# Kernel tuning notes

Hardware: AMD Instinct MI355X
Metric: run time of the kernel (lower is better)

The kernel has to match this reference:

```python
import jax, jax.numpy as jnp
import numpy as np

D = 64        # embedding_dim
H = 16        # embedding_dim // 4
DAY = 86400.0
N_USERS = 200000
T_TOTAL = 8400000


def _mlp(x, w1, b1, w2, b2):
    return jax.nn.relu(x @ w1 + b1) @ w2 + b2


def setup_inputs() -> dict:
    key = jax.random.key(0)
    ks = jax.random.split(key, 20)
    N, T = N_USERS, T_TOTAL
    # every user gets >= 3 check-ins, rest assigned randomly
    base = np.tile(np.arange(N, dtype=np.int32), 3)
    rnd = np.asarray(jax.random.randint(ks[0], (T - 3 * N,), 0, N, dtype=jnp.int32))
    segment_ids = jnp.asarray(np.sort(np.concatenate([base, rnd])).astype(np.int32))
    # quantized coordinates so per-user unique-row counting is meaningful
    locations = jnp.round(jax.random.normal(ks[1], (T, 2), jnp.float32) * 50.0) / 50.0
    timestamps = jax.random.uniform(ks[2], (T,), jnp.float32, 0.0, 1.0e7)
    categories = jax.random.randint(ks[3], (T,), 0, 10, dtype=jnp.int32)

    def lin(k, din, dout):
        kw, kb = jax.random.split(k)
        w = jax.random.normal(kw, (din, dout), jnp.float32) / np.float32(np.sqrt(din))
        b = jax.random.normal(kb, (dout,), jnp.float32) * 0.01
        return w, b

    p = {}
    ki = 4
    for nm, din in [("loc", 2), ("tmp", 3), ("act", 10), ("mob", 4)]:
        p[f"w_{nm}1"], p[f"b_{nm}1"] = lin(ks[ki], din, H); ki += 1
        p[f"w_{nm}2"], p[f"b_{nm}2"] = lin(ks[ki], H, H); ki += 1
    p["w_cmb1"], p["b_cmb1"] = lin(ks[ki], D, D); ki += 1
    p["w_cmb2"], p["b_cmb2"] = lin(ks[ki], D, D)
    return dict(locations=locations, timestamps=timestamps,
                categories=categories, segment_ids=segment_ids, num_users=N, **p)


def reference(locations, timestamps,
              w_loc1, b_loc1, w_loc2, b_loc2,
              w_tmp1, b_tmp1, w_tmp2, b_tmp2,
              w_act1, b_act1, w_act2, b_act2,
              w_mob1, b_mob1, w_mob2, b_mob2,
              w_cmb1, b_cmb1, w_cmb2, b_cmb2,
              categories, segment_ids, num_users):
    seg, N = segment_ids, num_users
    ss = lambda v: jax.ops.segment_sum(v, seg, num_segments=N, indices_are_sorted=True)
    L = ss(jnp.ones_like(timestamps))                        # [N] check-ins per user

    # home location = mean over user's locations
    home = ss(locations) / L[:, None]                        # [N, 2]

    # temporal patterns: mean hour / day / month
    hours = jnp.mod(timestamps, DAY) / 3600.0
    days = jnp.mod(timestamps / DAY, 7.0)
    months = jnp.mod(timestamps / (30.0 * DAY), 12.0)
    tmp = ss(jnp.stack([hours, days, months], -1)) / L[:, None]   # [N, 3]

    # activity distribution over 10 POI categories
    hist = jnp.zeros((N, 10), locations.dtype).at[seg, categories].add(1.0)
    hs = hist.sum(-1, keepdims=True)
    act = jnp.where(hs > 0, hist / jnp.maximum(hs, 1.0), hist)    # [N, 10]

    # mobility stats: radius = std (ddof=1) of distance to centroid
    d = jnp.linalg.norm(locations - home[seg], axis=1)
    dmean = ss(d) / L
    radius = jnp.sqrt(ss((d - dmean[seg]) ** 2) / (L - 1.0))

    # diversity: unique locations per user via segment-local lexsort
    x, y = locations[:, 0], locations[:, 1]
    order = jnp.lexsort((y, x, seg))
    sx, sy, sseg = x[order], y[order], seg[order]
    new = jnp.concatenate([jnp.ones((1,), bool),
                           (sseg[1:] != sseg[:-1]) | (sx[1:] != sx[:-1]) | (sy[1:] != sy[:-1])])
    uniq = jax.ops.segment_sum(new.astype(locations.dtype), sseg,
                               num_segments=N, indices_are_sorted=True)
    diversity = uniq / L

    # frequency: check-ins per day of time span
    tmax = jax.ops.segment_max(timestamps, seg, num_segments=N, indices_are_sorted=True)
    tmin = jax.ops.segment_min(timestamps, seg, num_segments=N, indices_are_sorted=True)
    span = (tmax - tmin) / DAY
    freq = L / jnp.maximum(span, 1.0)

    # regularity: 1 / (std(consecutive time diffs, ddof=1) + 1e-6)
    diffs = timestamps[1:] - timestamps[:-1]
    same = seg[1:] == seg[:-1]
    seg1 = seg[1:]
    ss1 = lambda v: jax.ops.segment_sum(v, seg1, num_segments=N, indices_are_sorted=True)
    m = L - 1.0                                              # diffs per user
    dmu = ss1(jnp.where(same, diffs, 0.0)) / m
    dvar = ss1(jnp.where(same, (diffs - dmu[seg1]) ** 2, 0.0)) / (m - 1.0)
    reg = 1.0 / (jnp.sqrt(dvar) + 1e-6)

    mob = jnp.stack([radius, diversity, freq, reg], -1)      # [N, 4]

    feats = jnp.concatenate([
        _mlp(home, w_loc1, b_loc1, w_loc2, b_loc2),
        _mlp(tmp, w_tmp1, b_tmp1, w_tmp2, b_tmp2),
        _mlp(act, w_act1, b_act1, w_act2, b_act2),
        _mlp(mob, w_mob1, b_mob1, w_mob2, b_mob2),
    ], -1)                                                   # [N, 64]
    return _mlp(feats, w_cmb1, b_cmb1, w_cmb2, b_cmb2)       # [N, 64]
```

## Files before the change

kernel.cpp:

```cpp
#include <hip/hip_runtime.h>

typedef short bf16x8 __attribute__((ext_vector_type(8)));
typedef float f32x4 __attribute__((ext_vector_type(4)));

struct Params {
  const float* loc; const float* ts; const int* cat; const int* seg;
  const int* off;
  const float *wl1,*bl1,*wl2,*bl2;
  const float *wt1,*bt1,*wt2,*bt2;
  const float *wa1,*ba1,*wa2,*ba2;
  const float *wm1,*bm1,*wm2,*bm2;
  const float *wc1,*bc1,*wc2,*bc2;
  float* out;
  unsigned* wfrag;
  int N, T, use_off;
};

__global__ void offsets_kernel(const int* __restrict__ seg, int* __restrict__ off, int T, int N) {
  int i = blockIdx.x * blockDim.x + threadIdx.x;
  if (i == 0) off[N] = T;
  if (i < T) {
    int s = seg[i];
    if (i == 0 || seg[i-1] != s) off[s] = i;
  }
}

__device__ __forceinline__ int rdlane_i(int v, int l) {
  return __builtin_amdgcn_readlane(v, l);
}

__device__ __forceinline__ unsigned bf16r(float f) {
  unsigned x = __float_as_uint(f);
  return (x + 0x7fffu + ((x >> 16) & 1u)) >> 16;
}
__device__ __forceinline__ unsigned pack_hl(float f) {
  unsigned hi = bf16r(f);
  float r = f - __uint_as_float(hi << 16);
  return (hi << 16) | bf16r(r);
}

__device__ __forceinline__ float exact_fmod(float a, float m, float rcp_m) {
  float q = floorf(a * rcp_m);
  float r = fmaf(q, -m, a);
  if (r < 0.0f) r += m;
  else if (r >= m) r -= m;
  return r;
}

__device__ __forceinline__ f32x4 mfma16(bf16x8 a, bf16x8 b, f32x4 c) {
  return __builtin_amdgcn_mfma_f32_16x16x32_bf16(a, b, c, 0, 0, 0);
}

__device__ __forceinline__ void lda(const unsigned* rp, bf16x8& hi, bf16x8& lo) {
  uint4 w0 = *(const uint4*)rp;
  uint4 w1 = *(const uint4*)(rp + 4);
  union { unsigned u[4]; bf16x8 v; } H, L;
  H.u[0] = __builtin_amdgcn_perm(w0.y, w0.x, 0x07060302u);
  H.u[1] = __builtin_amdgcn_perm(w0.w, w0.z, 0x07060302u);
  H.u[2] = __builtin_amdgcn_perm(w1.y, w1.x, 0x07060302u);
  H.u[3] = __builtin_amdgcn_perm(w1.w, w1.z, 0x07060302u);
  L.u[0] = __builtin_amdgcn_perm(w0.y, w0.x, 0x05040100u);
  L.u[1] = __builtin_amdgcn_perm(w0.w, w0.z, 0x05040100u);
  L.u[2] = __builtin_amdgcn_perm(w1.y, w1.x, 0x05040100u);
  L.u[3] = __builtin_amdgcn_perm(w1.w, w1.z, 0x05040100u);
  hi = H.v; lo = L.v;
}

__device__ __forceinline__ float bdval_(const float* wl2, const float* wt2,
                                        const float* wa2, const float* wm2,
                                        int k, int col) {
  if ((k >> 4) != (col >> 4)) return 0.f;
  int b = col >> 4;
  const float* W2 = (b & 2) ? ((b & 1) ? wm2 : wa2) : ((b & 1) ? wt2 : wl2);
  return W2[(k & 15) * 16 + (col & 15)];
}

__device__ __forceinline__ unsigned frag_word(const Params& p, int m) {
  int fi = m >> 8;
  int ln = (m >> 2) & 63;
  int j2 = m & 3;
  int layer, nt, ks;
  if (fi < 4)       { layer = 0; nt = fi;             ks = nt >> 1; }
  else if (fi < 12) { layer = 1; nt = (fi - 4) >> 1;  ks = (fi - 4) & 1; }
  else              { layer = 2; nt = (fi - 12) >> 1; ks = (fi - 12) & 1; }
  int col = nt * 16 + (ln & 15);
  int k0  = ks * 32 + ((ln >> 4) << 3) + (j2 << 1);
  float v0, v1;
  if (layer == 0) {
    v0 = bdval_(p.wl2, p.wt2, p.wa2, p.wm2, k0, col);
    v1 = bdval_(p.wl2, p.wt2, p.wa2, p.wm2, k0 + 1, col);
  } else {
    const float* W = (layer == 1) ? p.wc1 : p.wc2;
    v0 = W[k0 * 64 + col]; v1 = W[(k0 + 1) * 64 + col];
  }
  return (bf16r(v1) << 16) | bf16r(v0);
}

__global__ void pack_kernel(Params p) {
  int m = blockIdx.x * 256 + threadIdx.x;
  if (m < 5120) p.wfrag[m] = frag_word(p, m);
}

__device__ __forceinline__ bf16x8 g_ldb(const Params& p, int fi, int lane) {
  union { uint4 q; unsigned u[4]; bf16x8 v; } U;
  if (p.wfrag) {
    U.q = *(const uint4*)(p.wfrag + ((fi * 64 + lane) << 2));
  } else {
    int m = fi * 256 + lane * 4;
    U.u[0] = frag_word(p, m + 0);
    U.u[1] = frag_word(p, m + 1);
    U.u[2] = frag_word(p, m + 2);
    U.u[3] = frag_word(p, m + 3);
  }
  return U.v;
}

__device__ __forceinline__ int lower_bound(const int* seg, int T, int v) {
  int lo = 0, hi = T;
  while (lo < hi) { int m = (lo + hi) >> 1; if (seg[m] < v) lo = m + 1; else hi = m; }
  return lo;
}

__device__ __forceinline__ float pscan_f(float v) {
  v += __int_as_float(__builtin_amdgcn_update_dpp(0, __float_as_int(v), 0x111, 0xf, 0xf, true));
  v += __int_as_float(__builtin_amdgcn_update_dpp(0, __float_as_int(v), 0x112, 0xf, 0xf, true));
  v += __int_as_float(__builtin_amdgcn_update_dpp(0, __float_as_int(v), 0x114, 0xf, 0xf, true));
  v += __int_as_float(__builtin_amdgcn_update_dpp(0, __float_as_int(v), 0x118, 0xf, 0xf, true));
  v += __int_as_float(__builtin_amdgcn_update_dpp(0, __float_as_int(v), 0x142, 0xa, 0xf, true));
  v += __int_as_float(__builtin_amdgcn_update_dpp(0, __float_as_int(v), 0x143, 0xc, 0xf, true));
  return v;
}
__device__ __forceinline__ unsigned pscan_u(unsigned v) {
  int x = (int)v;
  x += __builtin_amdgcn_update_dpp(0, x, 0x111, 0xf, 0xf, true);
  x += __builtin_amdgcn_update_dpp(0, x, 0x112, 0xf, 0xf, true);
  x += __builtin_amdgcn_update_dpp(0, x, 0x114, 0xf, 0xf, true);
  x += __builtin_amdgcn_update_dpp(0, x, 0x118, 0xf, 0xf, true);
  x += __builtin_amdgcn_update_dpp(0, x, 0x142, 0xa, 0xf, true);
  x += __builtin_amdgcn_update_dpp(0, x, 0x143, 0xc, 0xf, true);
  return (unsigned)x;
}
__device__ __forceinline__ unsigned wshr1_u(unsigned v) {
  return (unsigned)__builtin_amdgcn_update_dpp(0, (int)v, 0x138, 0xf, 0xf, true);
}
__device__ __forceinline__ float wshr1_f(float v) {
  return __int_as_float(__builtin_amdgcn_update_dpp(0, __float_as_int(v), 0x138, 0xf, 0xf, true));
}

#define DPPI0(v, ctrl, rm) __builtin_amdgcn_update_dpp(0, (v), ctrl, rm, 0xf, true)
#define DPPFO(v, o, ctrl, rm) __int_as_float(__builtin_amdgcn_update_dpp(__float_as_int(o), __float_as_int(v), ctrl, rm, 0xf, false))

struct Conds { bool c1,c2,c4,c8,cA,cB; };
__device__ __forceinline__ Conds mkconds(int lane, int dist) {
  Conds C;
  C.c1 = dist >= 1; C.c2 = dist >= 2; C.c4 = dist >= 4; C.c8 = dist >= 8;
  C.cA = ((lane & 15) + 1) <= dist;
  C.cB = (lane - 31) <= dist;
  return C;
}
__device__ __forceinline__ int smaxi(int v) {
  int i;
  i = DPPI0(v,0x111,0xf); v = max(v,i);
  i = DPPI0(v,0x112,0xf); v = max(v,i);
  i = DPPI0(v,0x114,0xf); v = max(v,i);
  i = DPPI0(v,0x118,0xf); v = max(v,i);
  i = DPPI0(v,0x142,0xa); v = max(v,i);
  i = DPPI0(v,0x143,0xc); v = max(v,i);
  return v;
}
__device__ __forceinline__ float smaxf(float v, const Conds& C) {
  const float NI = __int_as_float(0xff800000u);
  float i;
  i = DPPFO(v,NI,0x111,0xf); v = C.c1 ? fmaxf(v,i) : v;
  i = DPPFO(v,NI,0x112,0xf); v = C.c2 ? fmaxf(v,i) : v;
  i = DPPFO(v,NI,0x114,0xf); v = C.c4 ? fmaxf(v,i) : v;
  i = DPPFO(v,NI,0x118,0xf); v = C.c8 ? fmaxf(v,i) : v;
  i = DPPFO(v,NI,0x142,0xa); v = C.cA ? fmaxf(v,i) : v;
  i = DPPFO(v,NI,0x143,0xc); v = C.cB ? fmaxf(v,i) : v;
  return v;
}
__device__ __forceinline__ float sminf(float v, const Conds& C) {
  const float PI_ = __int_as_float(0x7f800000u);
  float i;
  i = DPPFO(v,PI_,0x111,0xf); v = C.c1 ? fminf(v,i) : v;
  i = DPPFO(v,PI_,0x112,0xf); v = C.c2 ? fminf(v,i) : v;
  i = DPPFO(v,PI_,0x114,0xf); v = C.c4 ? fminf(v,i) : v;
  i = DPPFO(v,PI_,0x118,0xf); v = C.c8 ? fminf(v,i) : v;
  i = DPPFO(v,PI_,0x142,0xa); v = C.cA ? fminf(v,i) : v;
  i = DPPFO(v,PI_,0x143,0xc); v = C.cB ? fminf(v,i) : v;
  return v;
}

__global__ __launch_bounds__(256, 4) void mobility_kernel(Params p) {
  __shared__ __align__(16) unsigned s_pool[4352];
  __shared__ float s_w1[304];
  __shared__ float s_b1[64], s_b2[64], s_bc1[64], s_bc2[64];

  int tid = threadIdx.x;
  int lane = tid & 63, w = tid >> 6;

  if (tid < 32)  s_w1[tid]       = p.wl1[tid];
  if (tid < 48)  s_w1[32 + tid]  = p.wt1[tid];
  if (tid < 160) s_w1[80 + tid]  = p.wa1[tid];
  if (tid < 64)  s_w1[240 + tid] = p.wm1[tid];
  if (tid < 16) {
    s_b1[tid]    = p.bl1[tid]; s_b1[16+tid] = p.bt1[tid];
    s_b1[32+tid] = p.ba1[tid]; s_b1[48+tid] = p.bm1[tid];
    s_b2[tid]    = p.bl2[tid]; s_b2[16+tid] = p.bt2[tid];
    s_b2[32+tid] = p.ba2[tid]; s_b2[48+tid] = p.bm2[tid];
  }
  if (tid < 64) { s_bc1[tid] = p.bc1[tid]; s_bc2[tid] = p.bc2[tid]; }
  __syncthreads();

  int uw0 = blockIdx.x * 64 + w * 16;
  if (uw0 >= p.N) return;
  int myu = uw0 + lane;
  int myuc = min(myu, p.N - 1);
  int s0, e0;
  if (p.use_off) {
    s0 = p.off[myuc]; e0 = p.off[myuc + 1];
  } else {
    s0 = lower_bound(p.seg, p.T, myuc);
    e0 = lower_bound(p.seg, p.T, myuc + 1);
  }
  int W0 = rdlane_i(s0, 0);
  int W1 = rdlane_i(e0, 15);
  float Lf = (float)(e0 - s0);

  const float2* lp2 = (const float2*)p.loc;
  const float NINF = __int_as_float(0xff800000u);
  const float PINF = __int_as_float(0x7f800000u);

  int aKx = 0, aKy = 0, aXX = 0;
  float aH = 0.f, aDY = 0.f, aT = 0.f, aDF2 = 0.f;
  unsigned aH0 = 0u, aH1 = 0u, aH2 = 0u;
  float aTMX = NINF, aTMN = PINF;

  for (int base = W0; base < W1; base += 64) {
    int e = base + lane;
    bool on = e < W1;
    int ec = on ? e : (W1 - 1);
    int sv = p.seg[ec];
    int sp = (ec > 0) ? p.seg[ec - 1] : -1;
    int sn = (ec + 1 < p.T) ? p.seg[ec + 1] : -2;
    float t  = p.ts[ec];
    float tnx = (ec + 1 < p.T) ? p.ts[ec + 1] : 0.f;
    int c = p.cat[ec];
    float2 xy = lp2[ec];

    unsigned vXY = 0u, vXX = 0u, vH0 = 0u, vH1 = 0u, vH2 = 0u;
    float vH = 0.f, vDY = 0.f, vT = 0.f, vDF2 = 0.f;
    float vtmx = NINF, vtmn = PINF;
    if (on) {
      int kx = (int)lrintf(xy.x * 50.0f);
      int ky = (int)lrintf(xy.y * 50.0f);
      vXY = ((unsigned)(kx + 512) << 16) | (unsigned)(ky + 512);
      vXX = (unsigned)(kx * kx + ky * ky);
      float hr = exact_fmod(t, 86400.0f, 1.0f / 86400.0f);
      vH = hr * (1.0f / 3600.0f);
      float ud = (float)((double)t * (1.0 / 86400.0));
      vDY = exact_fmod(ud, 7.0f, 1.0f / 7.0f);
      vT = t;
      unsigned bit = 1u << ((c & 3) * 8);
      int wsel = c >> 2;
      vH0 = (wsel == 0) ? bit : 0u;
      vH1 = (wsel == 1) ? bit : 0u;
      vH2 = (wsel == 2) ? bit : 0u;
      if (sn == sv) { float dt = tnx - t; vDF2 = dt * dt; }
      vtmx = t; vtmn = t;
    }

    unsigned pXY = pscan_u(vXY), pXX = pscan_u(vXX);
    unsigned pH0 = pscan_u(vH0), pH1 = pscan_u(vH1), pH2 = pscan_u(vH2);
    float pH = pscan_f(vH), pDY = pscan_f(vDY), pT = pscan_f(vT), pDF2 = pscan_f(vDF2);

    bool head = (!on) || (sp != sv);
    int j = smaxi(head ? lane : 0);
    Conds C = mkconds(lane, lane - j);
    float pTMX = smaxf(vtmx, C);
    float pTMN = sminf(vtmn, C);

    int lo = min(max(s0 - base, 0), 64);
    int hi = min(max(e0 - base, 0), 64);
    int idx = max(hi - 1, 0);
    unsigned PXY = (unsigned)__shfl((int)pXY, idx);
    unsigned PXX = (unsigned)__shfl((int)pXX, idx);
    unsigned PH0 = (unsigned)__shfl((int)pH0, idx);
    unsigned PH1 = (unsigned)__shfl((int)pH1, idx);
    unsigned PH2 = (unsigned)__shfl((int)pH2, idx);
    float PH = __shfl(pH, idx), PDY = __shfl(pDY, idx);
    float PT = __shfl(pT, idx), PDF2 = __shfl(pDF2, idx);
    float PTMX = __shfl(pTMX, idx), PTMN = __shfl(pTMN, idx);
    unsigned LXY = wshr1_u(PXY), LXX = wshr1_u(PXX);
    unsigned LH0 = wshr1_u(PH0), LH1 = wshr1_u(PH1), LH2 = wshr1_u(PH2);
    float LH = wshr1_f(PH), LDY = wshr1_f(PDY);
    float LT = wshr1_f(PT), LDF2 = wshr1_f(PDF2);

    if (hi > lo) {
      int cnt = hi - lo;
      bool ul_ = lo > 0;
      unsigned dXY = PXY - (ul_ ? LXY : 0u);
      aKx += (int)(dXY >> 16) - (cnt << 9);
      aKy += (int)(dXY & 0xffffu) - (cnt << 9);
      aXX += (int)(PXX - (ul_ ? LXX : 0u));
      aH0 += PH0 - (ul_ ? LH0 : 0u);
      aH1 += PH1 - (ul_ ? LH1 : 0u);
      aH2 += PH2 - (ul_ ? LH2 : 0u);
      aH   += PH   - (ul_ ? LH   : 0.f);
      aDY  += PDY  - (ul_ ? LDY  : 0.f);
      aT   += PT   - (ul_ ? LT   : 0.f);
      aDF2 += PDF2 - (ul_ ? LDF2 : 0.f);
      aTMX = fmaxf(aTMX, PTMX);
      aTMN = fminf(aTMN, PTMN);
    }
  }

  float hx, hy;
  {
    float sx = (float)aKx / 50.0f, sy = (float)aKy / 50.0f;
    hx = sx / Lf; hy = sy / Lf;
  }

  float aD = 0.f;
  for (int base = W0; base < W1; base += 64) {
    int e = base + lane;
    bool on = e < W1;
    int ec = on ? e : (W1 - 1);
    int sv = p.seg[ec];
    float2 xy = lp2[ec];
    int ul = sv - uw0;
    float hxu = __shfl(hx, ul), hyu = __shfl(hy, ul);
    float d = 0.f;
    if (on) {
      float dx = xy.x - hxu, dyv = xy.y - hyu;
      d = sqrtf(fmaf(dx, dx, dyv * dyv));
    }
    float pD = pscan_f(d);
    int lo = min(max(s0 - base, 0), 64);
    int hi = min(max(e0 - base, 0), 64);
    int idx = max(hi - 1, 0);
    float PD = __shfl(pD, idx);
    float LD = wshr1_f(PD);
    if (hi > lo) aD += PD - ((lo > 0) ? LD : 0.f);
  }

  unsigned* fw = s_pool + w * 1088;
  unsigned* hashp = fw;
  float uqf = 0.f;
  for (int uu = 0; uu < 16; ++uu) {
    if (uw0 + uu >= p.N) break;
    int suu = rdlane_i(s0, uu), euu = rdlane_i(e0, uu);
    int Lu = euu - suu;
    int uq = 0;
    if (Lu <= 96) {
      hashp[lane] = 0u; hashp[64 + lane] = 0u;
      asm volatile("s_waitcnt lgkmcnt(0)" ::: "memory");
      for (int b2 = suu; b2 < euu; b2 += 64) {
        int i = b2 + lane;
        bool fresh = false;
        if (i < euu) {
          float2 xy = lp2[i];
          int kx = (int)lrintf(xy.x * 50.0f) + 2048;
          int ky = (int)lrintf(xy.y * 50.0f) + 2048;
          unsigned key = (((unsigned)kx << 12) | (unsigned)ky) + 1u;
          unsigned h = (key * 2654435761u) >> 25;
          while (true) {
            unsigned old = atomicCAS(&hashp[h], 0u, key);
            if (old == 0u) { fresh = true; break; }
            if (old == key) break;
            h = (h + 1) & 127u;
          }
        }
        uq += (int)__popcll(__ballot(fresh));
      }
    } else {
      for (int b2 = suu; b2 < euu; b2 += 64) {
        int i = b2 + lane;
        bool fresh = false;
        if (i < euu) {
          float x = p.loc[2*(size_t)i], y = p.loc[2*(size_t)i+1];
          fresh = true;
          for (int jj = suu; jj < i; ++jj) {
            if (p.loc[2*(size_t)jj] == x && p.loc[2*(size_t)jj+1] == y) { fresh = false; break; }
          }
        }
        uq += (int)__popcll(__ballot(fresh));
      }
    }
    if (lane == uu) uqf = (float)uq;
  }
  asm volatile("s_waitcnt lgkmcnt(0)" ::: "memory");

  int lr = lane & 15, g2 = lane >> 4;
  int us0 = __shfl(s0, lr), ue0 = __shfl(e0, lr);
  float LfU = (float)(ue0 - us0);
  int KX = __shfl(aKx, lr), KY = __shfl(aKy, lr), XX = __shfl(aXX, lr);
  float H_ = __shfl(aH, lr), DY_ = __shfl(aDY, lr);
  float T_ = __shfl(aT, lr), DF2_ = __shfl(aDF2, lr);
  unsigned H0_ = (unsigned)__shfl((int)aH0, lr);
  unsigned H1_ = (unsigned)__shfl((int)aH1, lr);
  unsigned H2_ = (unsigned)__shfl((int)aH2, lr);
  float TMX_ = __shfl(aTMX, lr), TMN_ = __shfl(aTMN, lr);
  float D_ = __shfl(aD, lr), UQ_ = __shfl(uqf, lr);

  unsigned hp16[16];
  if (g2 == 0) {
    float sxU = (float)KX / 50.0f, syU = (float)KY / 50.0f;
    float hxU = sxU / LfU, hyU = syU / LfU;
    #pragma unroll
    for (int j = 0; j < 16; ++j)
      hp16[j] = pack_hl(fmaxf(s_b1[j] + hxU * s_w1[j] + hyU * s_w1[16 + j], 0.f));
  } else if (g2 == 1) {
    float th = H_ / LfU, tdy = DY_ / LfU;
    float tmo = (T_ * (1.0f / 2592000.0f)) / LfU;
    #pragma unroll
    for (int j = 0; j < 16; ++j)
      hp16[j] = pack_hl(fmaxf(s_b1[16 + j] + th * s_w1[32 + j] + tdy * s_w1[48 + j]
                              + tmo * s_w1[64 + j], 0.f));
  } else if (g2 == 2) {
    float act[10];
    act[0] = (float)(H0_ & 255u) / LfU;
    act[1] = (float)((H0_ >> 8) & 255u) / LfU;
    act[2] = (float)((H0_ >> 16) & 255u) / LfU;
    act[3] = (float)((H0_ >> 24) & 255u) / LfU;
    act[4] = (float)(H1_ & 255u) / LfU;
    act[5] = (float)((H1_ >> 8) & 255u) / LfU;
    act[6] = (float)((H1_ >> 16) & 255u) / LfU;
    act[7] = (float)((H1_ >> 24) & 255u) / LfU;
    act[8] = (float)(H2_ & 255u) / LfU;
    act[9] = (float)((H2_ >> 8) & 255u) / LfU;
    #pragma unroll
    for (int j = 0; j < 16; ++j) {
      float aa = s_b1[32 + j];
      #pragma unroll
      for (int b = 0; b < 10; ++b) aa = fmaf(act[b], s_w1[80 + b * 16 + j], aa);
      hp16[j] = pack_hl(fmaxf(aa, 0.f));
    }
  } else {
    float sxU = (float)KX / 50.0f, syU = (float)KY / 50.0f;
    float sxx = (float)XX / 2500.0f;
    float sD = D_;
    float sD2 = sxx - (sxU * sxU + syU * syU) / LfU;
    float varD = (sD2 - sD * sD / LfU) / (LfU - 1.0f);
    float rad  = sqrtf(fmaxf(varD, 0.0f));
    float divy = UQ_ / LfU;
    float span = (TMX_ - TMN_) / 86400.0f;
    float freq = LfU / fmaxf(span, 1.0f);
    float tfirst = p.ts[us0];
    float tlast  = p.ts[ue0 - 1];
    float sdf = tlast - tfirst;
    float mm   = LfU - 1.0f;
    float dmu  = sdf / mm;
    float dvar = (DF2_ - mm * dmu * dmu) / (mm - 1.0f);
    float reg  = 1.0f / (sqrtf(fmaxf(dvar, 0.0f)) + 1e-6f);
    #pragma unroll
    for (int j = 0; j < 16; ++j)
      hp16[j] = pack_hl(fmaxf(s_b1[48 + j] + rad * s_w1[240 + j] + divy * s_w1[256 + j]
                              + freq * s_w1[272 + j] + reg * s_w1[288 + j], 0.f));
  }

  {
    unsigned* row = fw + lr * 68 + g2 * 16;
    #pragma unroll
    for (int j = 0; j < 4; ++j)
      *(uint4*)(row + 4 * j) = make_uint4(hp16[4*j], hp16[4*j+1], hp16[4*j+2], hp16[4*j+3]);
  }
  asm volatile("s_waitcnt lgkmcnt(0)" ::: "memory");

  int lg = lane >> 4;
  const unsigned* arow = fw + lr * 68 + (lg << 3);

  bf16x8 ah[2], al[2];
  lda(arow,      ah[0], al[0]);
  lda(arow + 32, ah[1], al[1]);
  f32x4 acc[4];
  #pragma unroll
  for (int nt = 0; nt < 4; ++nt) {
    float bv = s_b2[nt * 16 + lr];
    acc[nt] = (f32x4){bv, bv, bv, bv};
    int ks = nt >> 1;
    bf16x8 bw = g_ldb(p, nt, lane);
    acc[nt] = mfma16(ah[ks], bw, acc[nt]);
    acc[nt] = mfma16(al[ks], bw, acc[nt]);
  }
  #pragma unroll
  for (int nt = 0; nt < 4; ++nt)
    #pragma unroll
    for (int r = 0; r < 4; ++r)
      fw[(lg * 4 + r) * 68 + nt * 16 + lr] = pack_hl(acc[nt][r]);
  asm volatile("s_waitcnt lgkmcnt(0)" ::: "memory");

  lda(arow,      ah[0], al[0]);
  lda(arow + 32, ah[1], al[1]);
  #pragma unroll
  for (int nt = 0; nt < 4; ++nt) {
    float bv = s_bc1[nt * 16 + lr];
    acc[nt] = (f32x4){bv, bv, bv, bv};
    #pragma unroll
    for (int ks = 0; ks < 2; ++ks) {
      bf16x8 bw = g_ldb(p, 4 + nt * 2 + ks, lane);
      acc[nt] = mfma16(ah[ks], bw, acc[nt]);
      acc[nt] = mfma16(al[ks], bw, acc[nt]);
    }
  }
  #pragma unroll
  for (int nt = 0; nt < 4; ++nt)
    #pragma unroll
    for (int r = 0; r < 4; ++r)
      fw[(lg * 4 + r) * 68 + nt * 16 + lr] = pack_hl(fmaxf(acc[nt][r], 0.f));
  asm volatile("s_waitcnt lgkmcnt(0)" ::: "memory");

  lda(arow,      ah[0], al[0]);
  lda(arow + 32, ah[1], al[1]);
  #pragma unroll
  for (int nt = 0; nt < 4; ++nt) {
    float bv = s_bc2[nt * 16 + lr];
    acc[nt] = (f32x4){bv, bv, bv, bv};
    #pragma unroll
    for (int ks = 0; ks < 2; ++ks) {
      bf16x8 bw = g_ldb(p, 12 + nt * 2 + ks, lane);
      acc[nt] = mfma16(ah[ks], bw, acc[nt]);
      acc[nt] = mfma16(al[ks], bw, acc[nt]);
    }
  }
  #pragma unroll
  for (int nt = 0; nt < 4; ++nt)
    #pragma unroll
    for (int r = 0; r < 4; ++r) {
      int uo = uw0 + lg * 4 + r;
      if (uo < p.N) p.out[(size_t)uo * 64 + nt * 16 + lr] = acc[nt][r];
    }
}

extern "C" void kernel_launch(void* const* d_in, const int* in_sizes, int n_in,
                              void* d_out, int out_size, void* d_ws, size_t ws_size,
                              hipStream_t stream) {
  Params p;
  p.loc = (const float*)d_in[0];
  p.ts  = (const float*)d_in[1];
  p.cat = (const int*)d_in[2];
  p.seg = (const int*)d_in[3];
  p.wl1 = (const float*)d_in[5];  p.bl1 = (const float*)d_in[6];
  p.wl2 = (const float*)d_in[7];  p.bl2 = (const float*)d_in[8];
  p.wt1 = (const float*)d_in[9];  p.bt1 = (const float*)d_in[10];
  p.wt2 = (const float*)d_in[11]; p.bt2 = (const float*)d_in[12];
  p.wa1 = (const float*)d_in[13]; p.ba1 = (const float*)d_in[14];
  p.wa2 = (const float*)d_in[15]; p.ba2 = (const float*)d_in[16];
  p.wm1 = (const float*)d_in[17]; p.bm1 = (const float*)d_in[18];
  p.wm2 = (const float*)d_in[19]; p.bm2 = (const float*)d_in[20];
  p.wc1 = (const float*)d_in[21]; p.bc1 = (const float*)d_in[22];
  p.wc2 = (const float*)d_in[23]; p.bc2 = (const float*)d_in[24];
  p.out = (float*)d_out;
  p.N = out_size / 64;
  p.T = in_sizes[1];
  int* off = (int*)d_ws;
  p.off = off;
  p.use_off = (ws_size >= (size_t)(p.N + 1) * sizeof(int)) ? 1 : 0;

  size_t fragOff = (((size_t)p.N + 1) + 3) & ~(size_t)3;
  p.wfrag = nullptr;
  if (ws_size >= (fragOff + 5120) * sizeof(unsigned)) {
    p.wfrag = (unsigned*)d_ws + fragOff;
    pack_kernel<<<20, 256, 0, stream>>>(p);
  }

  if (p.use_off) {
    offsets_kernel<<<(p.T + 255)/256, 256, 0, stream>>>(p.seg, off, p.T, p.N);
  }
  int nblocks = (p.N + 63) / 64;
  mobility_kernel<<<nblocks, 256, 0, stream>>>(p);
}
```

Measured before the change: 181.2 us.

## Fold segment min/max and distance sum into per-user unique-count loop

Drops the segmented DPP max/min scans from the main pass and removes the separate distance pass. Per-user timestamp min/max and distance-to-home sums are now accumulated inside the per-user hashing loop, followed by a butterfly reduction per user. This saves one full pass over locations and the segmented-scan instructions. In exchange it adds a 64-lane xor-shuffle reduction per user, and each user's work is now serialised over the 16 users of a wave, which can leave lanes idle for short users.

Measured after the change: 177.0 us. 2.3% less time.

```diff
diff --git a/kernel.cpp b/kernel.cpp
--- a/kernel.cpp
+++ b/kernel.cpp
@@ -27,6 +27,9 @@
 
 __device__ __forceinline__ int rdlane_i(int v, int l) {
   return __builtin_amdgcn_readlane(v, l);
+}
+__device__ __forceinline__ float rdlane_f(float v, int l) {
+  return __int_as_float(__builtin_amdgcn_readlane(__float_as_int(v), l));
 }
 
 __device__ __forceinline__ unsigned bf16r(float f) {
@@ -147,50 +150,6 @@
   return __int_as_float(__builtin_amdgcn_update_dpp(0, __float_as_int(v), 0x138, 0xf, 0xf, true));
 }
 
-#define DPPI0(v, ctrl, rm) __builtin_amdgcn_update_dpp(0, (v), ctrl, rm, 0xf, true)
-#define DPPFO(v, o, ctrl, rm) __int_as_float(__builtin_amdgcn_update_dpp(__float_as_int(o), __float_as_int(v), ctrl, rm, 0xf, false))
-
-struct Conds { bool c1,c2,c4,c8,cA,cB; };
-__device__ __forceinline__ Conds mkconds(int lane, int dist) {
-  Conds C;
-  C.c1 = dist >= 1; C.c2 = dist >= 2; C.c4 = dist >= 4; C.c8 = dist >= 8;
-  C.cA = ((lane & 15) + 1) <= dist;
-  C.cB = (lane - 31) <= dist;
-  return C;
-}
-__device__ __forceinline__ int smaxi(int v) {
-  int i;
-  i = DPPI0(v,0x111,0xf); v = max(v,i);
-  i = DPPI0(v,0x112,0xf); v = max(v,i);
-  i = DPPI0(v,0x114,0xf); v = max(v,i);
-  i = DPPI0(v,0x118,0xf); v = max(v,i);
-  i = DPPI0(v,0x142,0xa); v = max(v,i);
-  i = DPPI0(v,0x143,0xc); v = max(v,i);
-  return v;
-}
-__device__ __forceinline__ float smaxf(float v, const Conds& C) {
-  const float NI = __int_as_float(0xff800000u);
-  float i;
-  i = DPPFO(v,NI,0x111,0xf); v = C.c1 ? fmaxf(v,i) : v;
-  i = DPPFO(v,NI,0x112,0xf); v = C.c2 ? fmaxf(v,i) : v;
-  i = DPPFO(v,NI,0x114,0xf); v = C.c4 ? fmaxf(v,i) : v;
-  i = DPPFO(v,NI,0x118,0xf); v = C.c8 ? fmaxf(v,i) : v;
-  i = DPPFO(v,NI,0x142,0xa); v = C.cA ? fmaxf(v,i) : v;
-  i = DPPFO(v,NI,0x143,0xc); v = C.cB ? fmaxf(v,i) : v;
-  return v;
-}
-__device__ __forceinline__ float sminf(float v, const Conds& C) {
-  const float PI_ = __int_as_float(0x7f800000u);
-  float i;
-  i = DPPFO(v,PI_,0x111,0xf); v = C.c1 ? fminf(v,i) : v;
-  i = DPPFO(v,PI_,0x112,0xf); v = C.c2 ? fminf(v,i) : v;
-  i = DPPFO(v,PI_,0x114,0xf); v = C.c4 ? fminf(v,i) : v;
-  i = DPPFO(v,PI_,0x118,0xf); v = C.c8 ? fminf(v,i) : v;
-  i = DPPFO(v,PI_,0x142,0xa); v = C.cA ? fminf(v,i) : v;
-  i = DPPFO(v,PI_,0x143,0xc); v = C.cB ? fminf(v,i) : v;
-  return v;
-}
-
 __global__ __launch_bounds__(256, 4) void mobility_kernel(Params p) {
   __shared__ __align__(16) unsigned s_pool[4352];
   __shared__ float s_w1[304];
@@ -234,14 +193,12 @@
   int aKx = 0, aKy = 0, aXX = 0;
   float aH = 0.f, aDY = 0.f, aT = 0.f, aDF2 = 0.f;
   unsigned aH0 = 0u, aH1 = 0u, aH2 = 0u;
-  float aTMX = NINF, aTMN = PINF;
 
   for (int base = W0; base < W1; base += 64) {
     int e = base + lane;
     bool on = e < W1;
     int ec = on ? e : (W1 - 1);
     int sv = p.seg[ec];
-    int sp = (ec > 0) ? p.seg[ec - 1] : -1;
     int sn = (ec + 1 < p.T) ? p.seg[ec + 1] : -2;
     float t  = p.ts[ec];
     float tnx = (ec + 1 < p.T) ? p.ts[ec + 1] : 0.f;
@@ -250,7 +207,6 @@
 
     unsigned vXY = 0u, vXX = 0u, vH0 = 0u, vH1 = 0u, vH2 = 0u;
     float vH = 0.f, vDY = 0.f, vT = 0.f, vDF2 = 0.f;
-    float vtmx = NINF, vtmn = PINF;
     if (on) {
       int kx = (int)lrintf(xy.x * 50.0f);
       int ky = (int)lrintf(xy.y * 50.0f);
@@ -267,18 +223,11 @@
       vH1 = (wsel == 1) ? bit : 0u;
       vH2 = (wsel == 2) ? bit : 0u;
       if (sn == sv) { float dt = tnx - t; vDF2 = dt * dt; }
-      vtmx = t; vtmn = t;
     }
 
     unsigned pXY = pscan_u(vXY), pXX = pscan_u(vXX);
     unsigned pH0 = pscan_u(vH0), pH1 = pscan_u(vH1), pH2 = pscan_u(vH2);
     float pH = pscan_f(vH), pDY = pscan_f(vDY), pT = pscan_f(vT), pDF2 = pscan_f(vDF2);
-
-    bool head = (!on) || (sp != sv);
-    int j = smaxi(head ? lane : 0);
-    Conds C = mkconds(lane, lane - j);
-    float pTMX = smaxf(vtmx, C);
-    float pTMN = sminf(vtmn, C);
 
     int lo = min(max(s0 - base, 0), 64);
     int hi = min(max(e0 - base, 0), 64);
@@ -290,7 +239,6 @@
     unsigned PH2 = (unsigned)__shfl((int)pH2, idx);
     float PH = __shfl(pH, idx), PDY = __shfl(pDY, idx);
     float PT = __shfl(pT, idx), PDF2 = __shfl(pDF2, idx);
-    float PTMX = __shfl(pTMX, idx), PTMN = __shfl(pTMN, idx);
     unsigned LXY = wshr1_u(PXY), LXX = wshr1_u(PXX);
     unsigned LH0 = wshr1_u(PH0), LH1 = wshr1_u(PH1), LH2 = wshr1_u(PH2);
     float LH = wshr1_f(PH), LDY = wshr1_f(PDY);
@@ -310,8 +258,6 @@
       aDY  += PDY  - (ul_ ? LDY  : 0.f);
       aT   += PT   - (ul_ ? LT   : 0.f);
       aDF2 += PDF2 - (ul_ ? LDF2 : 0.f);
-      aTMX = fmaxf(aTMX, PTMX);
-      aTMN = fminf(aTMN, PTMN);
     }
   }
 
@@ -321,37 +267,16 @@
     hx = sx / Lf; hy = sy / Lf;
   }
 
-  float aD = 0.f;
-  for (int base = W0; base < W1; base += 64) {
-    int e = base + lane;
-    bool on = e < W1;
-    int ec = on ? e : (W1 - 1);
-    int sv = p.seg[ec];
-    float2 xy = lp2[ec];
-    int ul = sv - uw0;
-    float hxu = __shfl(hx, ul), hyu = __shfl(hy, ul);
-    float d = 0.f;
-    if (on) {
-      float dx = xy.x - hxu, dyv = xy.y - hyu;
-      d = sqrtf(fmaf(dx, dx, dyv * dyv));
-    }
-    float pD = pscan_f(d);
-    int lo = min(max(s0 - base, 0), 64);
-    int hi = min(max(e0 - base, 0), 64);
-    int idx = max(hi - 1, 0);
-    float PD = __shfl(pD, idx);
-    float LD = wshr1_f(PD);
-    if (hi > lo) aD += PD - ((lo > 0) ? LD : 0.f);
-  }
-
   unsigned* fw = s_pool + w * 1088;
   unsigned* hashp = fw;
-  float uqf = 0.f;
+  float uqf = 0.f, tmxA = NINF, tmnA = PINF, aD = 0.f;
   for (int uu = 0; uu < 16; ++uu) {
     if (uw0 + uu >= p.N) break;
     int suu = rdlane_i(s0, uu), euu = rdlane_i(e0, uu);
+    float hxu = rdlane_f(hx, uu), hyu = rdlane_f(hy, uu);
     int Lu = euu - suu;
     int uq = 0;
+    float cmx = NINF, cmn = PINF, dsum = 0.f;
     if (Lu <= 96) {
       hashp[lane] = 0u; hashp[64 + lane] = 0u;
       asm volatile("s_waitcnt lgkmcnt(0)" ::: "memory");
@@ -359,7 +284,11 @@
         int i = b2 + lane;
         bool fresh = false;
         if (i < euu) {
+          float tv = p.ts[i];
+          cmx = fmaxf(cmx, tv); cmn = fminf(cmn, tv);
           float2 xy = lp2[i];
+          float dx = xy.x - hxu, dyv = xy.y - hyu;
+          dsum += sqrtf(fmaf(dx, dx, dyv * dyv));
           int kx = (int)lrintf(xy.x * 50.0f) + 2048;
           int ky = (int)lrintf(xy.y * 50.0f) + 2048;
           unsigned key = (((unsigned)kx << 12) | (unsigned)ky) + 1u;
@@ -378,7 +307,11 @@
         int i = b2 + lane;
         bool fresh = false;
         if (i < euu) {
+          float tv = p.ts[i];
+          cmx = fmaxf(cmx, tv); cmn = fminf(cmn, tv);
           float x = p.loc[2*(size_t)i], y = p.loc[2*(size_t)i+1];
+          float dx = x - hxu, dyv = y - hyu;
+          dsum += sqrtf(fmaf(dx, dx, dyv * dyv));
           fresh = true;
           for (int jj = suu; jj < i; ++jj) {
             if (p.loc[2*(size_t)jj] == x && p.loc[2*(size_t)jj+1] == y) { fresh = false; break; }
@@ -387,7 +320,13 @@
         uq += (int)__popcll(__ballot(fresh));
       }
     }
-    if (lane == uu) uqf = (float)uq;
+    #pragma unroll
+    for (int o = 32; o > 0; o >>= 1) {
+      cmx = fmaxf(cmx, __shfl_xor(cmx, o));
+      cmn = fminf(cmn, __shfl_xor(cmn, o));
+      dsum += __shfl_xor(dsum, o);
+    }
+    if (lane == uu) { uqf = (float)uq; tmxA = cmx; tmnA = cmn; aD = dsum; }
   }
   asm volatile("s_waitcnt lgkmcnt(0)" ::: "memory");
 
@@ -400,7 +339,7 @@
   unsigned H0_ = (unsigned)__shfl((int)aH0, lr);
   unsigned H1_ = (unsigned)__shfl((int)aH1, lr);
   unsigned H2_ = (unsigned)__shfl((int)aH2, lr);
-  float TMX_ = __shfl(aTMX, lr), TMN_ = __shfl(aTMN, lr);
+  float TMX_ = __shfl(tmxA, lr), TMN_ = __shfl(tmnA, lr);
   float D_ = __shfl(aD, lr), UQ_ = __shfl(uqf, lr);
 
   unsigned hp16[16];
```
